# Optimization experiments

Hardware: AMD Instinct MI355X
Metric: run time of the kernel (lower is better)

Reference implementation:

```python
import jax, jax.numpy as jnp
import numpy as np


def _ln(x, g, b, eps=1e-5):
    m = x.mean(-1, keepdims=True)
    v = x.var(-1, keepdims=True)
    return (x - m) / jnp.sqrt(v + eps) * g + b


def setup_inputs() -> dict:
    key = jax.random.key(0)
    ks = jax.random.split(key, 12)
    B, N, F, D, DI = 1024, 100000, 128, 256, 512

    def w(k, shape, fan_in):
        return jax.random.normal(k, shape, jnp.float32) / np.sqrt(fan_in).astype(np.float32)

    return {
        "x_num": jax.random.normal(ks[0], (B, F), jnp.float32),
        "cand_num": jax.random.normal(ks[1], (N, F), jnp.float32),
        "cand_y": jax.random.normal(ks[2], (N, 1), jnp.float32),
        "W_lin": w(ks[3], (F, D), F), "b_lin": jnp.zeros(D, jnp.float32),
        "W_K": w(ks[4], (D, D), D), "b_K": jnp.zeros(D, jnp.float32),
        "W_Y": w(ks[5], (1, D), 2), "b_Y": jnp.zeros(D, jnp.float32),
        "W_T1": w(ks[6], (D, DI), D), "b_T1": jnp.zeros(DI, jnp.float32),
        "W_T2": w(ks[7], (DI, D), DI),
        "ln_p_g": jnp.ones(D, jnp.float32), "ln_p_b": jnp.zeros(D, jnp.float32),
        "W_P1": w(ks[8], (D, DI), D), "b_P1": jnp.zeros(DI, jnp.float32),
        "W_P2": w(ks[9], (DI, D), DI), "b_P2": jnp.zeros(D, jnp.float32),
        "ln_o_g": jnp.ones(D, jnp.float32), "ln_o_b": jnp.zeros(D, jnp.float32),
        "W_out": w(ks[10], (D, 1), D), "b_out": jnp.zeros(1, jnp.float32),
        "context_size": 96,
    }


def reference(x_num, cand_num, cand_y,
              W_lin, b_lin, W_K, b_K, W_Y, b_Y,
              W_T1, b_T1, W_T2,
              ln_p_g, ln_p_b, W_P1, b_P1, W_P2, b_P2,
              ln_o_g, ln_o_b, W_out, b_out,
              context_size):
    # Encoder (encoder_n_blocks=0, normlization=None -> identity f)
    x_enc = x_num @ W_lin + b_lin                       # [B, D]
    k = x_enc @ W_K + b_K                               # [B, D]
    # Candidate keys (computed under torch.no_grad in the original)
    ki_all = jax.lax.stop_gradient((cand_num @ W_lin + b_lin) @ W_K + b_K)  # [N, D]

    # Exact brute-force L2 kNN == faiss.IndexFlatL2
    d2 = (k * k).sum(-1, keepdims=True) - 2.0 * (k @ ki_all.T) + (ki_all * ki_all).sum(-1)  # [B, N]
    _, I = jax.lax.top_k(-d2, context_size)             # [B, C] ascending distance
    ki = ki_all[I]                                      # [B, C, D]

    # S = ||k - ki||^2 per the source formula; softmax over context
    S = (k * k).sum(-1, keepdims=True) \
        - 2.0 * jnp.einsum('bd,bcd->bc', k, ki) \
        + (ki * ki).sum(-1)                             # [B, C]
    weights = jax.nn.softmax(S, axis=-1)                # context_dropout=0 (eval)

    encode_y = cand_y[I] @ W_Y + b_Y                    # [B, C, D]
    diff = k[:, None, :] - ki                           # [B, C, D]
    V = encode_y + jax.nn.relu(diff @ W_T1 + b_T1) @ W_T2  # T MLP, no bias on 2nd linear
    V = jnp.einsum('bc,bcd->bd', weights, V)            # weighted context reduction

    x = x_enc + V
    # predictor residual block: LN -> Linear -> ReLU -> Linear
    h = _ln(x, ln_p_g, ln_p_b)
    x = x + (jax.nn.relu(h @ W_P1 + b_P1) @ W_P2 + b_P2)
    # head P: LN -> ReLU -> Linear(d, 1)
    return jax.nn.relu(_ln(x, ln_o_g, ln_o_b)) @ W_out + b_out  # [B, 1]
```

## Files before the change

### kernel.cpp

```cpp
#include <hip/hip_runtime.h>
#include <math.h>

#define BQ 1024
#define FDIM 128
#define DDIM 256
#define DIDIM 512
#define NTOT 100000
#define NP 100096
#define CTX 96
#define CAP 8192
#define MSUB 12288
#define RSUB 48
#define LBUF 1536
#define CSTR 16

typedef _Float16 f16x8 __attribute__((ext_vector_type(8)));
typedef _Float16 f16x4 __attribute__((ext_vector_type(4)));
typedef _Float16 f16x2 __attribute__((ext_vector_type(2)));
typedef float f32x4 __attribute__((ext_vector_type(4)));

__global__ __launch_bounds__(256) void k_fuse(
    const float* __restrict__ Wlin, const float* __restrict__ blin,
    const float* __restrict__ WK, const float* __restrict__ bK,
    float* __restrict__ Wf, float* __restrict__ bf)
{
    __shared__ float red[256];
    int i = blockIdx.x, j = threadIdx.x;
    if (i < FDIM) {
        float acc = 0.f;
        for (int l = 0; l < DDIM; ++l) acc += Wlin[i*DDIM + l] * WK[l*DDIM + j];
        Wf[i*DDIM + j] = acc;
    } else {
        float acc = bK[j];
        for (int l = 0; l < DDIM; ++l) acc += blin[l] * WK[l*DDIM + j];
        bf[j] = acc;
        red[j] = acc*acc; __syncthreads();
        for (int s2 = 128; s2 > 0; s2 >>= 1) { if (j < s2) red[j] += red[j+s2]; __syncthreads(); }
        if (j == 0) bf[256] = red[0];
    }
}

__global__ __launch_bounds__(256) void k_fuse2(
    const float* __restrict__ Wf, const float* __restrict__ WT1, float* __restrict__ WfT1)
{
    __shared__ float wr[DDIM];
    int i = blockIdx.x, j = threadIdx.x;
    wr[j] = Wf[i*DDIM + j];
    __syncthreads();
    float a0 = 0.f, a1 = 0.f;
    for (int l = 0; l < DDIM; ++l) {
        float w = wr[l];
        a0 += w * WT1[(size_t)l*DIDIM + j];
        a1 += w * WT1[(size_t)l*DIDIM + j + 256];
    }
    WfT1[(size_t)i*DIDIM + j] = a0;
    WfT1[(size_t)i*DIDIM + j + 256] = a1;
}

__global__ __launch_bounds__(128) void k_cvt_w(
    const float* __restrict__ Wf, const float* __restrict__ WfT1, _Float16* __restrict__ Wsp)
{
    int j = blockIdx.x, l = threadIdx.x;
    float w = (j < DDIM) ? Wf[l*DDIM + j] : WfT1[(size_t)l*DIDIM + (j - DDIM)];
    _Float16 h = (_Float16)w;
    float hf = (float)h;
    Wsp[(size_t)j*384 + l]       = h;
    Wsp[(size_t)j*384 + 128 + l] = (_Float16)((w - hf) * 64.f);
    Wsp[(size_t)j*384 + 256 + l] = (_Float16)(hf * 0.015625f);
}

__global__ __launch_bounds__(256) void k_query(
    const float* __restrict__ x, const float* __restrict__ Wlin,
    const float* __restrict__ blin, const float* __restrict__ Wf,
    const float* __restrict__ bf,
    float* __restrict__ xenc, float* __restrict__ kq)
{
    __shared__ float xs[FDIM];
    int b = blockIdx.x, j = threadIdx.x;
    if (j < FDIM) xs[j] = x[(size_t)b*FDIM + j];
    __syncthreads();
    float a0 = blin[j], a1 = bf[j];
    for (int l = 0; l < FDIM; ++l) {
        float xv = xs[l];
        a0 += xv * Wlin[l*DDIM + j];
        a1 += xv * Wf[l*DDIM + j];
    }
    xenc[(size_t)b*DDIM + j] = a0;
    kq[(size_t)b*DDIM + j] = a1;
}

__global__ __launch_bounds__(128) void k_kp(
    const float* __restrict__ kq, const float* __restrict__ Wf, float* __restrict__ kp)
{
    __shared__ float ks[DDIM];
    int b = blockIdx.x, l = threadIdx.x;
    ks[l] = kq[(size_t)b*DDIM + l];
    ks[l+128] = kq[(size_t)b*DDIM + l + 128];
    __syncthreads();
    float a = 0.f;
    for (int d = 0; d < DDIM; ++d) a += Wf[l*DDIM + d] * ks[d];
    kp[(size_t)b*FDIM + l] = a;
}

__global__ __launch_bounds__(256) void k_xp(
    const float* __restrict__ x, const float* __restrict__ WfT1,
    const float* __restrict__ bT1, float* __restrict__ xP)
{
    __shared__ float xs[FDIM];
    int b = blockIdx.x, j = threadIdx.x;
    if (j < FDIM) xs[j] = x[(size_t)b*FDIM + j];
    __syncthreads();
    float a0 = bT1[j], a1 = bT1[j + 256];
    for (int l = 0; l < FDIM; ++l) {
        float xv = xs[l];
        a0 += xv * WfT1[(size_t)l*DIDIM + j];
        a1 += xv * WfT1[(size_t)l*DIDIM + j + 256];
    }
    xP[(size_t)b*DIDIM + j] = a0;
    xP[(size_t)b*DIDIM + j + 256] = a1;
}

__global__ __launch_bounds__(256) void k_cvt_kp(
    const float* __restrict__ kp, _Float16* __restrict__ kp2)
{
    int t = blockIdx.x*256 + threadIdx.x;
    int row = t >> 5;
    int c4 = (t & 31) * 4;
    float4 v = *(const float4*)(kp + (size_t)row*FDIM + c4);
    float vv[4] = {v.x, v.y, v.z, v.w};
    f16x4 h, hs, l;
    #pragma unroll
    for (int q = 0; q < 4; ++q) {
        _Float16 hq = (_Float16)vv[q];
        float hf = (float)hq;
        h[q]  = hq;
        hs[q] = (_Float16)(hf * 0.015625f);
        l[q]  = (_Float16)((vv[q] - hf) * 64.f);
    }
    size_t b = (size_t)row*384 + c4;
    *(f16x4*)(kp2 + b)       = h;
    *(f16x4*)(kp2 + b + 128) = l;
    *(f16x4*)(kp2 + b + 256) = hs;
}

__global__ __launch_bounds__(256) void k_cvt_cand(
    const float* __restrict__ cand, _Float16* __restrict__ c2)
{
    int t = blockIdx.x*256 + threadIdx.x;
    int row = t >> 5;
    int c4 = (t & 31) * 4;
    float4 v = {0.f, 0.f, 0.f, 0.f};
    if (row < NTOT) v = *(const float4*)(cand + (size_t)row*FDIM + c4);
    float vv[4] = {v.x, v.y, v.z, v.w};
    f16x4 h, hs, l;
    #pragma unroll
    for (int q = 0; q < 4; ++q) {
        _Float16 hq = (_Float16)vv[q];
        float hf = (float)hq;
        h[q]  = hq;
        hs[q] = (_Float16)(hf * 0.015625f);
        l[q]  = (_Float16)((vv[q] - hf) * 64.f);
    }
    size_t b = (size_t)row*384 + c4;
    *(f16x4*)(c2 + b)       = h;
    *(f16x4*)(c2 + b + 128) = hs;
    *(f16x4*)(c2 + b + 256) = l;
}

__global__ __launch_bounds__(256) void k_cnorm(
    const _Float16* __restrict__ A, const _Float16* __restrict__ B,
    float* __restrict__ knp, const float* __restrict__ bf)
{
    __shared__ __align__(16) _Float16 As[128*64];
    __shared__ __align__(16) _Float16 Bs[128*64];
    int tid = threadIdx.x;
    int lane = tid & 63, wv = tid >> 6;
    int wm = wv >> 1, wn = wv & 1;
    int bn = blockIdx.x * 128;
    int bm = blockIdx.y * 128;
    f32x4 acc[4][4] = {};
    const size_t baseA = (size_t)bm * 384;
    const size_t baseB = (size_t)bn * 384;
    for (int kt = 0; kt < 6; ++kt) {
        #pragma unroll
        for (int r = 0; r < 4; ++r) {
            int w = wv*4 + r;
            int s = w*64 + lane;
            int rl = s & 15;
            int q  = (s >> 4) & 3;
            int kk2= (s >> 6) & 1;
            int ii = (s >> 7) & 3;
            int wq = (s >> 9) & 1;
            size_t goff = (size_t)(wq*64 + ii*16 + rl)*384 + kt*64 + (kk2*4 + q)*8;
            __builtin_amdgcn_global_load_lds(
                (const __attribute__((address_space(1))) void*)(A + baseA + goff),
                (__attribute__((address_space(3))) void*)(As + w*512), 16, 0, 0);
            __builtin_amdgcn_global_load_lds(
                (const __attribute__((address_space(1))) void*)(B + baseB + goff),
                (__attribute__((address_space(3))) void*)(Bs + w*512), 16, 0, 0);
        }
        __syncthreads();
        #pragma unroll
        for (int kk = 0; kk < 2; ++kk) {
            f16x8 af[4], bfr[4];
            #pragma unroll
            for (int i = 0; i < 4; ++i)
                af[i] = *(const f16x8*)&As[((wm*8 + i*2 + kk)*64 + (lane>>4)*16 + (lane&15))*8];
            #pragma unroll
            for (int j = 0; j < 4; ++j)
                bfr[j] = *(const f16x8*)&Bs[((wn*8 + j*2 + kk)*64 + (lane>>4)*16 + (lane&15))*8];
            #pragma unroll
            for (int i = 0; i < 4; ++i)
                #pragma unroll
                for (int j = 0; j < 4; ++j)
                    acc[i][j] = __builtin_amdgcn_mfma_f32_16x16x32_f16(af[i], bfr[j], acc[i][j], 0, 0, 0);
        }
        __syncthreads();
    }
    float bfv[4];
    #pragma unroll
    for (int j = 0; j < 4; ++j) bfv[j] = bf[bn + wn*64 + j*16 + (lane&15)];
    int bnt = bn >> 7;
    #pragma unroll
    for (int i = 0; i < 4; ++i) {
        #pragma unroll
        for (int rg = 0; rg < 4; ++rg) {
            float s = 0.f;
            #pragma unroll
            for (int j = 0; j < 4; ++j) {
                float q = acc[i][j][rg];
                s += q * (q + 2.f*bfv[j]);
            }
            s += __shfl_xor(s, 1, 64);
            s += __shfl_xor(s, 2, 64);
            s += __shfl_xor(s, 4, 64);
            s += __shfl_xor(s, 8, 64);
            if ((lane & 15) == 0) {
                int row = bm + wm*64 + i*16 + (lane>>4)*4 + rg;
                knp[(size_t)(bnt*2 + wn)*NP + row] = s;
            }
        }
    }
}

__global__ __launch_bounds__(256) void k_norm_fin(
    const float* __restrict__ knp, const float* __restrict__ bf, float* __restrict__ kinorm)
{
    int n = blockIdx.x*256 + threadIdx.x;
    kinorm[n] = (n < NTOT)
        ? bf[256] + knp[n] + knp[(size_t)NP + n] + knp[(size_t)2*NP + n] + knp[(size_t)3*NP + n]
        : INFINITY;
}

__global__ __launch_bounds__(256) void k_mini(
    const _Float16* __restrict__ kp2, const _Float16* __restrict__ cand2,
    const float* __restrict__ kinorm, _Float16* __restrict__ msb)
{
    __shared__ __align__(16) _Float16 As[128*64];
    __shared__ __align__(16) _Float16 Bs[128*64];
    int tid = threadIdx.x;
    int lane = tid & 63, wv = tid >> 6;
    int wm = wv >> 1, wn = wv & 1;
    int bm = blockIdx.x * 128;
    int bn = blockIdx.y * 128;
    f32x4 acc[4][4] = {};
    const size_t baseA = (size_t)bm * 384;
    const size_t baseB = (size_t)bn * 384;
    for (int kt = 0; kt < 2; ++kt) {
        #pragma unroll
        for (int r = 0; r < 4; ++r) {
            int w = wv*4 + r;
            int s = w*64 + lane;
            int rl = s & 15;
            int q  = (s >> 4) & 3;
            int kk2= (s >> 6) & 1;
            int ii = (s >> 7) & 3;
            int wq = (s >> 9) & 1;
            size_t goff = (size_t)(wq*64 + ii*16 + rl)*384 + kt*64 + (kk2*4 + q)*8;
            __builtin_amdgcn_global_load_lds(
                (const __attribute__((address_space(1))) void*)(kp2 + baseA + goff),
                (__attribute__((address_space(3))) void*)(As + w*512), 16, 0, 0);
            __builtin_amdgcn_global_load_lds(
                (const __attribute__((address_space(1))) void*)(cand2 + baseB + goff),
                (__attribute__((address_space(3))) void*)(Bs + w*512), 16, 0, 0);
        }
        __syncthreads();
        #pragma unroll
        for (int kk = 0; kk < 2; ++kk) {
            f16x8 af[4], bfr[4];
            #pragma unroll
            for (int i = 0; i < 4; ++i)
                af[i] = *(const f16x8*)&As[((wm*8 + i*2 + kk)*64 + (lane>>4)*16 + (lane&15))*8];
            #pragma unroll
            for (int j = 0; j < 4; ++j)
                bfr[j] = *(const f16x8*)&Bs[((wn*8 + j*2 + kk)*64 + (lane>>4)*16 + (lane&15))*8];
            #pragma unroll
            for (int i = 0; i < 4; ++i)
                #pragma unroll
                for (int j = 0; j < 4; ++j)
                    acc[i][j] = __builtin_amdgcn_mfma_f32_16x16x32_f16(af[i], bfr[j], acc[i][j], 0, 0, 0);
        }
        __syncthreads();
    }
    #pragma unroll
    for (int i = 0; i < 4; ++i) {
        int m = bm + wm*64 + i*16 + (lane>>4)*4;
        #pragma unroll
        for (int j = 0; j < 4; ++j) {
            int nl = bn + wn*64 + j*16 + (lane&15);
            float kn = kinorm[nl];
            #pragma unroll
            for (int rg = 0; rg < 4; ++rg)
                msb[(size_t)(m + rg)*MSUB + nl] = (_Float16)fmaxf(kn - 2.f*acc[i][j][rg], 0.f);
        }
    }
}

__global__ __launch_bounds__(256) void k_subT(
    const unsigned short* __restrict__ msb, int* __restrict__ Tq, int* __restrict__ cnt)
{
    __shared__ unsigned h[1024];
    __shared__ unsigned pr[256];
    __shared__ unsigned h2[64];
    __shared__ int tstar;
    __shared__ unsigned cbel;
    int b = blockIdx.x, tid = threadIdx.x;
    if (tid == 0) cnt[b*CSTR] = 0;
    #pragma unroll
    for (int i = 0; i < 4; ++i) h[tid + i*256] = 0;
    if (tid == 0) tstar = 1023;
    if (tid < 64) h2[tid] = 0;
    __syncthreads();
    const unsigned short* row = msb + (size_t)b*MSUB;
    for (int base = 0; base < MSUB; base += 2048) {
        uint4 u = *(const uint4*)(row + base + tid*8);
        atomicAdd(&h[(u.x & 0xffffu) >> 6], 1u);
        atomicAdd(&h[(u.x >> 16) >> 6], 1u);
        atomicAdd(&h[(u.y & 0xffffu) >> 6], 1u);
        atomicAdd(&h[(u.y >> 16) >> 6], 1u);
        atomicAdd(&h[(u.z & 0xffffu) >> 6], 1u);
        atomicAdd(&h[(u.z >> 16) >> 6], 1u);
        atomicAdd(&h[(u.w & 0xffffu) >> 6], 1u);
        atomicAdd(&h[(u.w >> 16) >> 6], 1u);
    }
    __syncthreads();
    unsigned s0 = h[tid*4], s1 = h[tid*4+1], s2 = h[tid*4+2], s3 = h[tid*4+3];
    unsigned tot = s0 + s1 + s2 + s3;
    pr[tid] = tot;
    __syncthreads();
    for (int off = 1; off < 256; off <<= 1) {
        unsigned t2 = (tid >= off) ? pr[tid - off] : 0;
        __syncthreads();
        pr[tid] += t2;
        __syncthreads();
    }
    unsigned c = pr[tid] - tot;
    int found = -1;
    c += s0; if (c >= RSUB) found = tid*4;
    if (found < 0) { c += s1; if (c >= RSUB) found = tid*4+1; }
    if (found < 0) { c += s2; if (c >= RSUB) found = tid*4+2; }
    if (found < 0) { c += s3; if (c >= RSUB) found = tid*4+3; }
    if (found >= 0) atomicMin(&tstar, found);
    __syncthreads();
    if (tid == (tstar >> 2)) {
        unsigned below = pr[tid] - tot;
        int pos = tstar & 3;
        if (pos > 0) below += s0;
        if (pos > 1) below += s1;
        if (pos > 2) below += s2;
        cbel = below;
    }
    __syncthreads();
    int ts = tstar;
    for (int base = 0; base < MSUB; base += 2048) {
        uint4 u = *(const uint4*)(row + base + tid*8);
        unsigned e[8] = { u.x & 0xffffu, u.x >> 16, u.y & 0xffffu, u.y >> 16,
                          u.z & 0xffffu, u.z >> 16, u.w & 0xffffu, u.w >> 16 };
        #pragma unroll
        for (int q = 0; q < 8; ++q)
            if ((int)(e[q] >> 6) == ts) atomicAdd(&h2[e[q] & 63], 1u);
    }
    __syncthreads();
    if (tid == 0) {
        unsigned cum = cbel; int code = 63;
        for (int i = 0; i < 64; ++i) { cum += h2[i]; if (cum >= RSUB) { code = i; break; } }
        Tq[b] = (ts << 6) + code;
    }
}

__global__ __launch_bounds__(256) void k_dist_mfma(
    const _Float16* __restrict__ kp2, const _Float16* __restrict__ cand2,
    const float* __restrict__ kinorm, const int* __restrict__ Tq,
    int* __restrict__ cnt, int* __restrict__ candI)
{
    __shared__ __align__(16) _Float16 As[128*64];
    __shared__ __align__(16) _Float16 Bs[128*64];
    __shared__ int lcnt;
    __shared__ unsigned lbuf[LBUF];
    int tid = threadIdx.x;
    int lane = tid & 63, wv = tid >> 6;
    int wm = wv >> 1, wn = wv & 1;
    int r0 = blockIdx.x & 7, u0 = blockIdx.x >> 3;
    int pq = r0*782 + u0;
    int bm = (pq & 7) * 128;
    int bn = (pq >> 3) * 128;
    if (tid == 0) lcnt = 0;
    f32x4 acc[4][4] = {};
    const size_t baseA = (size_t)bm * 384;
    const size_t baseB = (size_t)bn * 384;
    for (int kt = 0; kt < 2; ++kt) {
        #pragma unroll
        for (int r = 0; r < 4; ++r) {
            int w = wv*4 + r;
            int s = w*64 + lane;
            int rl = s & 15;
            int q  = (s >> 4) & 3;
            int kk2= (s >> 6) & 1;
            int ii = (s >> 7) & 3;
            int wq = (s >> 9) & 1;
            size_t goff = (size_t)(wq*64 + ii*16 + rl)*384 + kt*64 + (kk2*4 + q)*8;
            __builtin_amdgcn_global_load_lds(
                (const __attribute__((address_space(1))) void*)(kp2 + baseA + goff),
                (__attribute__((address_space(3))) void*)(As + w*512), 16, 0, 0);
            __builtin_amdgcn_global_load_lds(
                (const __attribute__((address_space(1))) void*)(cand2 + baseB + goff),
                (__attribute__((address_space(3))) void*)(Bs + w*512), 16, 0, 0);
        }
        __syncthreads();
        #pragma unroll
        for (int kk = 0; kk < 2; ++kk) {
            f16x8 af[4], bfr[4];
            #pragma unroll
            for (int i = 0; i < 4; ++i)
                af[i] = *(const f16x8*)&As[((wm*8 + i*2 + kk)*64 + (lane>>4)*16 + (lane&15))*8];
            #pragma unroll
            for (int j = 0; j < 4; ++j)
                bfr[j] = *(const f16x8*)&Bs[((wn*8 + j*2 + kk)*64 + (lane>>4)*16 + (lane&15))*8];
            #pragma unroll
            for (int i = 0; i < 4; ++i)
                #pragma unroll
                for (int j = 0; j < 4; ++j)
                    acc[i][j] = __builtin_amdgcn_mfma_f32_16x16x32_f16(af[i], bfr[j], acc[i][j], 0, 0, 0);
        }
        __syncthreads();
    }
    #pragma unroll
    for (int i = 0; i < 4; ++i) {
        int m0 = bm + wm*64 + i*16 + (lane>>4)*4;
        int tqs[4];
        #pragma unroll
        for (int rg = 0; rg < 4; ++rg) tqs[rg] = Tq[m0 + rg];
        #pragma unroll
        for (int j = 0; j < 4; ++j) {
            int nl = bn + wn*64 + j*16 + (lane&15);
            float kn = kinorm[nl];
            #pragma unroll
            for (int rg = 0; rg < 4; ++rg) {
                float sc = fmaxf(kn - 2.f*acc[i][j][rg], 0.f);
                _Float16 k16 = (_Float16)sc;
                unsigned short kb;
                __builtin_memcpy(&kb, &k16, 2);
                if (kb <= (unsigned short)tqs[rg]) {
                    int p = atomicAdd(&lcnt, 1);
                    if (p < LBUF) lbuf[p] = ((unsigned)(m0 + rg) << 17) | (unsigned)nl;
                    else {
                        int pp = atomicAdd(&cnt[(m0 + rg)*CSTR], 1);
                        if (pp < CAP) candI[(size_t)(m0 + rg)*CAP + pp] = nl;
                    }
                }
            }
        }
    }
    __syncthreads();
    int c = lcnt < LBUF ? lcnt : LBUF;
    for (int i2 = tid; i2 < c; i2 += 256) {
        unsigned pk = lbuf[i2];
        int row = pk >> 17, col = (int)(pk & 0x1ffffu);
        int pp = atomicAdd(&cnt[row*CSTR], 1);
        if (pp < CAP) candI[(size_t)row*CAP + pp] = col;
    }
}

__device__ __forceinline__ float row_score(
    const float* __restrict__ cand, const float* kps, const float* __restrict__ kinorm, int n)
{
    float acc0 = 0.f, acc1 = 0.f;
    #pragma unroll 4
    for (int d = 0; d < FDIM; d += 8) {
        float4 v0 = *(const float4*)(cand + (size_t)n*FDIM + d);
        float4 v1 = *(const float4*)(cand + (size_t)n*FDIM + d + 4);
        acc0 += v0.x*kps[d]   + v0.y*kps[d+1] + v0.z*kps[d+2] + v0.w*kps[d+3];
        acc1 += v1.x*kps[d+4] + v1.y*kps[d+5] + v1.z*kps[d+6] + v1.w*kps[d+7];
    }
    return kinorm[n] - 2.f*(acc0 + acc1);
}

__global__ __launch_bounds__(256) void k_fix(
    const float* __restrict__ kp, const float* __restrict__ cand,
    const float* __restrict__ kinorm, int* __restrict__ cnt, int* __restrict__ candI)
{
    __shared__ float kps[FDIM];
    __shared__ unsigned h[1024];
    __shared__ unsigned pr[256];
    __shared__ unsigned h2[64];
    __shared__ int tstar;
    __shared__ unsigned cbel;
    __shared__ unsigned Tsh;
    int b = blockIdx.x, tid = threadIdx.x;
    int c0 = cnt[b*CSTR];
    if (c0 >= CTX && c0 <= CAP) return;
    if (tid < FDIM) kps[tid] = kp[(size_t)b*FDIM + tid];
    #pragma unroll
    for (int i = 0; i < 4; ++i) h[tid + i*256] = 0;
    if (tid == 0) tstar = 1023;
    if (tid < 64) h2[tid] = 0;
    __syncthreads();
    for (int n = tid; n < NTOT; n += 256) {
        float sc = fmaxf(row_score(cand, kps, kinorm, n), 0.f);
        _Float16 k16 = (_Float16)sc;
        unsigned short kb; __builtin_memcpy(&kb, &k16, 2);
        atomicAdd(&h[kb >> 6], 1u);
    }
    __syncthreads();
    unsigned s0 = h[tid*4], s1 = h[tid*4+1], s2 = h[tid*4+2], s3 = h[tid*4+3];
    unsigned tot = s0 + s1 + s2 + s3;
    pr[tid] = tot;
    __syncthreads();
    for (int off = 1; off < 256; off <<= 1) {
        unsigned t2 = (tid >= off) ? pr[tid - off] : 0;
        __syncthreads();
        pr[tid] += t2;
        __syncthreads();
    }
    unsigned c = pr[tid] - tot;
    int found = -1;
    c += s0; if (c >= CTX) found = tid*4;
    if (found < 0) { c += s1; if (c >= CTX) found = tid*4+1; }
    if (found < 0) { c += s2; if (c >= CTX) found = tid*4+2; }
    if (found < 0) { c += s3; if (c >= CTX) found = tid*4+3; }
    if (found >= 0) atomicMin(&tstar, found);
    __syncthreads();
    if (tid == (tstar >> 2)) {
        unsigned below = pr[tid] - tot;
        int pos = tstar & 3;
        if (pos > 0) below += s0;
        if (pos > 1) below += s1;
        if (pos > 2) below += s2;
        cbel = below;
    }
    __syncthreads();
    int ts = tstar;
    for (int n = tid; n < NTOT; n += 256) {
        float sc = fmaxf(row_score(cand, kps, kinorm, n), 0.f);
        _Float16 k16 = (_Float16)sc;
        unsigned short kb; __builtin_memcpy(&kb, &k16, 2);
        if ((int)((unsigned)kb >> 6) == ts) atomicAdd(&h2[kb & 63], 1u);
    }
    __syncthreads();
    if (tid == 0) {
        unsigned cum = cbel; int code = 63;
        for (int i = 0; i < 64; ++i) { cum += h2[i]; if (cum >= CTX) { code = i; break; } }
        Tsh = (unsigned)((ts << 6) + code);
        cnt[b*CSTR] = 0;
    }
    __syncthreads();
    unsigned T2 = Tsh;
    for (int n = tid; n < NTOT; n += 256) {
        float sc = fmaxf(row_score(cand, kps, kinorm, n), 0.f);
        _Float16 k16 = (_Float16)sc;
        unsigned short kb; __builtin_memcpy(&kb, &k16, 2);
        if ((unsigned)kb <= T2) {
            int pp = atomicAdd(&cnt[b*CSTR], 1);
            if (pp < CAP) candI[(size_t)b*CAP + pp] = n;
        }
    }
}

__global__ __launch_bounds__(256) void k_resc(
    const float* __restrict__ kp, const float* __restrict__ cand,
    const float* __restrict__ kinorm, const int* __restrict__ cnt,
    const int* __restrict__ candI,
    float* __restrict__ finV, int* __restrict__ finI)
{
    __shared__ float kps[FDIM];
    __shared__ float sval[2048];
    __shared__ int   sidx[2048];
    int b = blockIdx.x, tid = threadIdx.x;
    if (tid < FDIM) kps[tid] = kp[(size_t)b*FDIM + tid];
    if (tid < 128) { sval[tid] = INFINITY; sidx[tid] = 0x7fffffff; }
    int nc = cnt[b*CSTR]; if (nc > CAP) nc = CAP;
    __syncthreads();
    for (int c0 = 0; c0 < nc; c0 += 1920) {
        int m = nc - c0; if (m > 1920) m = 1920;
        for (int c = tid; c < m; c += 256) {
            int n = candI[(size_t)b*CAP + c0 + c];
            sval[128 + c] = row_score(cand, kps, kinorm, n);
            sidx[128 + c] = n;
        }
        __syncthreads();
        int nv = 128 + m;
        int size = 256; while (size < nv) size <<= 1;
        for (int i2 = nv + tid; i2 < size; i2 += 256) { sval[i2] = INFINITY; sidx[i2] = 0x7fffffff; }
        __syncthreads();
        for (int k2 = 2; k2 <= size; k2 <<= 1) {
            for (int jj = k2 >> 1; jj > 0; jj >>= 1) {
                for (int i = tid; i < size; i += 256) {
                    int ix = i ^ jj;
                    if (ix > i) {
                        bool up = ((i & k2) == 0);
                        float a = sval[i], b2 = sval[ix];
                        int ia = sidx[i], ib = sidx[ix];
                        bool gt = (a > b2) || (a == b2 && ia > ib);
                        if (gt == up) {
                            sval[i] = b2; sval[ix] = a;
                            sidx[i] = ib; sidx[ix] = ia;
                        }
                    }
                }
                __syncthreads();
            }
        }
    }
    if (tid < CTX) { finV[(size_t)b*CTX + tid] = sval[tid]; finI[(size_t)b*CTX + tid] = sidx[tid]; }
}

__global__ __launch_bounds__(128) void k_weights(
    const float* __restrict__ finV, const int* __restrict__ finI,
    const float* __restrict__ candy, float* __restrict__ wts, float* __restrict__ wy)
{
    __shared__ float sh[128];
    int b = blockIdx.x, t = threadIdx.x;
    float v = (t < CTX) ? finV[b*CTX + t] : -INFINITY;
    sh[t] = v; __syncthreads();
    for (int s2 = 64; s2 > 0; s2 >>= 1) { if (t < s2) sh[t] = fmaxf(sh[t], sh[t+s2]); __syncthreads(); }
    float m = sh[0]; __syncthreads();
    float e = (t < CTX) ? expf(v - m) : 0.f;
    sh[t] = e; __syncthreads();
    for (int s2 = 64; s2 > 0; s2 >>= 1) { if (t < s2) sh[t] += sh[t+s2]; __syncthreads(); }
    float w = e / sh[0]; __syncthreads();
    if (t < CTX) wts[b*CTX + t] = w;
    float yv = (t < CTX) ? candy[finI[b*CTX + t]] : 0.f;
    sh[t] = w * yv; __syncthreads();
    for (int s2 = 64; s2 > 0; s2 >>= 1) { if (t < s2) sh[t] += sh[t+s2]; __syncthreads(); }
    if (t == 0) wy[b] = sh[0];
}

__global__ __launch_bounds__(256) void k_tmlp2(
    const _Float16* __restrict__ c2, const _Float16* __restrict__ Wsp,
    const float* __restrict__ xP,
    const int* __restrict__ finI, const float* __restrict__ wts,
    float* __restrict__ Hw)
{
    __shared__ __align__(16) _Float16 As[768*8];
    __shared__ __align__(16) _Float16 Bs[1024*8];
    __shared__ int   idx[CTX];
    __shared__ float wsh[CTX];
    int b = blockIdx.x, ct = blockIdx.y;
    int tid = threadIdx.x;
    int lane = tid & 63, wv = tid >> 6;
    if (tid < CTX) { idx[tid] = finI[b*CTX + tid]; wsh[tid] = wts[b*CTX + tid]; }
    __syncthreads();
    f32x4 acc[6][2] = {};
    const _Float16* Wbase = Wsp + (size_t)(DDIM + ct*128) * 384;
    for (int kt = 0; kt < 2; ++kt) {
        #pragma unroll
        for (int w = 0; w < 3; ++w) {
            int s = (wv*3 + w)*64 + lane;
            int rl = s & 15, q = (s >> 4) & 3, kk2 = (s >> 6) & 1, ii = s >> 7;
            int grow = idx[ii*16 + rl];
            __builtin_amdgcn_global_load_lds(
                (const __attribute__((address_space(1))) void*)(c2 + (size_t)grow*384 + kt*64 + (kk2*4 + q)*8),
                (__attribute__((address_space(3))) void*)(As + (size_t)s*8), 16, 0, 0);
        }
        #pragma unroll
        for (int w = 0; w < 4; ++w) {
            int s = (wv*4 + w)*64 + lane;
            int rl = s & 15, q = (s >> 4) & 3, kk2 = (s >> 6) & 1, jj = s >> 7;
            __builtin_amdgcn_global_load_lds(
                (const __attribute__((address_space(1))) void*)(Wbase + (size_t)(jj*16 + rl)*384 + kt*64 + (kk2*4 + q)*8),
                (__attribute__((address_space(3))) void*)(Bs + (size_t)s*8), 16, 0, 0);
        }
        __syncthreads();
        #pragma unroll
        for (int kk = 0; kk < 2; ++kk) {
            f16x8 bfr[2];
            #pragma unroll
            for (int j = 0; j < 2; ++j)
                bfr[j] = *(const f16x8*)&Bs[(((wv*2 + j)*2 + kk)*64 + (lane>>4)*16 + (lane&15))*8];
            #pragma unroll
            for (int i = 0; i < 6; ++i) {
                f16x8 af = *(const f16x8*)&As[((i*2 + kk)*64 + (lane>>4)*16 + (lane&15))*8];
                #pragma unroll
                for (int j = 0; j < 2; ++j)
                    acc[i][j] = __builtin_amdgcn_mfma_f32_16x16x32_f16(af, bfr[j], acc[i][j], 0, 0, 0);
            }
        }
        __syncthreads();
    }
    #pragma unroll
    for (int j = 0; j < 2; ++j) {
        int col = ct*128 + wv*32 + j*16 + (lane & 15);
        float xv = xP[(size_t)b*DIDIM + col];
        float p = 0.f;
        #pragma unroll
        for (int i = 0; i < 6; ++i) {
            #pragma unroll
            for (int rg = 0; rg < 4; ++rg) {
                int row = i*16 + (lane>>4)*4 + rg;
                p += wsh[row] * fmaxf(xv - acc[i][j][rg], 0.f);
            }
        }
        p += __shfl_xor(p, 16, 64);
        p += __shfl_xor(p, 32, 64);
        if ((lane >> 4) == 0) Hw[(size_t)b*DIDIM + col] = p;
    }
}

__device__ __forceinline__ float bsum(float v, float* red, int j)
{
    red[j] = v; __syncthreads();
    if (j < 64) {
        float t = red[j] + red[j+64] + red[j+128] + red[j+192];
        #pragma unroll
        for (int o2 = 32; o2; o2 >>= 1) t += __shfl_xor(t, o2, 64);
        if (j == 0) red[0] = t;
    }
    __syncthreads();
    float t = red[0];
    __syncthreads();
    return t;
}

__global__ __launch_bounds__(256) void k_final4(
    const float* __restrict__ xenc, const float* __restrict__ Hw,
    const float* __restrict__ wy,
    const float* __restrict__ WY, const float* __restrict__ bY,
    const float* __restrict__ WT2,
    const float* __restrict__ lpg, const float* __restrict__ lpb,
    const float* __restrict__ WP1, const float* __restrict__ bP1,
    const float* __restrict__ WP2, const float* __restrict__ bP2,
    const float* __restrict__ logg, const float* __restrict__ lob,
    const float* __restrict__ Wout, const float* __restrict__ bout,
    float* __restrict__ out)
{
    __shared__ float hs[4][DIDIM];
    __shared__ float xs[4][DDIM];
    __shared__ float red[256];
    int b0 = blockIdx.x*4, j = threadIdx.x;
    #pragma unroll
    for (int r = 0; r < 4; ++r) {
        hs[r][j] = Hw[(size_t)(b0+r)*DIDIM + j];
        hs[r][j+256] = Hw[(size_t)(b0+r)*DIDIM + j + 256];
    }
    __syncthreads();
    float v[4];
    #pragma unroll
    for (int r = 0; r < 4; ++r) v[r] = wy[b0+r]*WY[j] + bY[j];
    for (int dd = 0; dd < DIDIM; ++dd) {
        float w = WT2[dd*DDIM + j];
        #pragma unroll
        for (int r = 0; r < 4; ++r) v[r] += hs[r][dd]*w;
    }
    float x[4];
    #pragma unroll
    for (int r = 0; r < 4; ++r) x[r] = xenc[(size_t)(b0+r)*DDIM + j] + v[r];
    #pragma unroll
    for (int r = 0; r < 4; ++r) {
        float mean = bsum(x[r], red, j) * (1.f/DDIM);
        float xc = x[r] - mean;
        float var = bsum(xc*xc, red, j) * (1.f/DDIM);
        float rstd = 1.f / sqrtf(var + 1e-5f);
        xs[r][j] = xc * rstd * lpg[j] + lpb[j];
    }
    __syncthreads();
    float u0[4], u1[4];
    #pragma unroll
    for (int r = 0; r < 4; ++r) { u0[r] = bP1[j]; u1[r] = bP1[j+256]; }
    for (int dd = 0; dd < DDIM; ++dd) {
        float w0 = WP1[(size_t)dd*DIDIM + j], w1 = WP1[(size_t)dd*DIDIM + j + 256];
        #pragma unroll
        for (int r = 0; r < 4; ++r) { float hd = xs[r][dd]; u0[r] += hd*w0; u1[r] += hd*w1; }
    }
    __syncthreads();
    #pragma unroll
    for (int r = 0; r < 4; ++r) { hs[r][j] = fmaxf(u0[r], 0.f); hs[r][j+256] = fmaxf(u1[r], 0.f); }
    __syncthreads();
    float x2[4];
    #pragma unroll
    for (int r = 0; r < 4; ++r) x2[r] = x[r] + bP2[j];
    for (int dd = 0; dd < DIDIM; ++dd) {
        float w = WP2[dd*DDIM + j];
        #pragma unroll
        for (int r = 0; r < 4; ++r) x2[r] += hs[r][dd]*w;
    }
    #pragma unroll
    for (int r = 0; r < 4; ++r) {
        float mean = bsum(x2[r], red, j) * (1.f/DDIM);
        float xc = x2[r] - mean;
        float var = bsum(xc*xc, red, j) * (1.f/DDIM);
        float rstd = 1.f / sqrtf(var + 1e-5f);
        float rr = fmaxf(xc * rstd * logg[j] + lob[j], 0.f);
        float s = bsum(rr * Wout[j], red, j);
        if (j == 0) out[b0+r] = s + bout[0];
    }
}

extern "C" void kernel_launch(void* const* d_in, const int* in_sizes, int n_in,
                              void* d_out, int out_size, void* d_ws, size_t ws_size,
                              hipStream_t stream)
{
    (void)in_sizes; (void)n_in; (void)out_size; (void)ws_size;
    const float* x_num = (const float*)d_in[0];
    const float* cand  = (const float*)d_in[1];
    const float* candy = (const float*)d_in[2];
    const float* Wlin  = (const float*)d_in[3];
    const float* blin  = (const float*)d_in[4];
    const float* WK    = (const float*)d_in[5];
    const float* bK    = (const float*)d_in[6];
    const float* WY    = (const float*)d_in[7];
    const float* bY    = (const float*)d_in[8];
    const float* WT1   = (const float*)d_in[9];
    const float* bT1   = (const float*)d_in[10];
    const float* WT2   = (const float*)d_in[11];
    const float* lpg   = (const float*)d_in[12];
    const float* lpb   = (const float*)d_in[13];
    const float* WP1   = (const float*)d_in[14];
    const float* bP1   = (const float*)d_in[15];
    const float* WP2   = (const float*)d_in[16];
    const float* bP2   = (const float*)d_in[17];
    const float* logg  = (const float*)d_in[18];
    const float* lob   = (const float*)d_in[19];
    const float* Wout  = (const float*)d_in[20];
    const float* bout  = (const float*)d_in[21];
    float* out = (float*)d_out;

    float* ws = (float*)d_ws;
    size_t o = 0;
    float* Wf     = ws + o; o += (size_t)FDIM*DDIM;
    float* bf     = ws + o; o += 320;
    float* WfT1   = ws + o; o += (size_t)FDIM*DIDIM;
    float* xenc   = ws + o; o += (size_t)BQ*DDIM;
    float* kq     = ws + o; o += (size_t)BQ*DDIM;
    float* kp     = ws + o; o += (size_t)BQ*FDIM;
    float* kinorm = ws + o; o += NP;
    float* knp    = ws + o; o += (size_t)4*NP;
    float* finV   = ws + o; o += (size_t)BQ*CTX;
    int*   finI   = (int*)(ws + o); o += (size_t)BQ*CTX;
    float* wts    = ws + o; o += (size_t)BQ*CTX;
    float* wy     = ws + o; o += BQ;
    int*   Tq     = (int*)(ws + o); o += BQ;
    float* Hw     = ws + o; o += (size_t)BQ*DIDIM;
    float* xP     = ws + o; o += (size_t)BQ*DIDIM;
    _Float16* kp2 = (_Float16*)(ws + o); o += (size_t)BQ*384/2;
    _Float16* c2  = (_Float16*)(ws + o); o += (size_t)NP*384/2;
    _Float16* Wsp = (_Float16*)(ws + o); o += (size_t)768*384/2;
    int*   cnt    = (int*)(ws + o); o += (size_t)BQ*CSTR;
    int*   candI  = (int*)(ws + o); o += (size_t)BQ*CAP;
    _Float16* msb = (_Float16*)(ws + o); o += (size_t)BQ*MSUB;

    k_fuse<<<dim3(FDIM+1), dim3(256), 0, stream>>>(Wlin, blin, WK, bK, Wf, bf);
    k_fuse2<<<dim3(FDIM), dim3(256), 0, stream>>>(Wf, WT1, WfT1);
    k_cvt_w<<<dim3(DDIM+DIDIM), dim3(128), 0, stream>>>(Wf, WfT1, Wsp);
    k_query<<<dim3(BQ), dim3(256), 0, stream>>>(x_num, Wlin, blin, Wf, bf, xenc, kq);
    k_kp<<<dim3(BQ), dim3(128), 0, stream>>>(kq, Wf, kp);
    k_xp<<<dim3(BQ), dim3(256), 0, stream>>>(x_num, WfT1, bT1, xP);
    k_cvt_kp<<<dim3(BQ*FDIM/4/256), dim3(256), 0, stream>>>(kp, kp2);
    k_cvt_cand<<<dim3(NP*FDIM/4/256), dim3(256), 0, stream>>>(cand, c2);

    k_cnorm<<<dim3(DDIM/128, NP/128), dim3(256), 0, stream>>>(c2, Wsp, knp, bf);
    k_norm_fin<<<dim3(NP/256), dim3(256), 0, stream>>>(knp, bf, kinorm);

    k_mini<<<dim3(BQ/128, MSUB/128), dim3(256), 0, stream>>>(kp2, c2, kinorm, msb);
    k_subT<<<dim3(BQ), dim3(256), 0, stream>>>((const unsigned short*)msb, Tq, cnt);

    k_dist_mfma<<<dim3((BQ/128)*(NP/128)), dim3(256), 0, stream>>>(kp2, c2, kinorm, Tq, cnt, candI);
    k_fix<<<dim3(BQ), dim3(256), 0, stream>>>(kp, cand, kinorm, cnt, candI);
    k_resc<<<dim3(BQ), dim3(256), 0, stream>>>(kp, cand, kinorm, cnt, candI, finV, finI);

    k_weights<<<dim3(BQ), dim3(128), 0, stream>>>(finV, finI, candy, wts, wy);

    k_tmlp2<<<dim3(BQ, 4), dim3(256), 0, stream>>>(c2, Wsp, xP, finI, wts, Hw);
    k_final4<<<dim3(BQ/4), dim3(256), 0, stream>>>(xenc, Hw, wy, WY, bY, WT2,
                                                   lpg, lpb, WP1, bP1, WP2, bP2,
                                                   logg, lob, Wout, bout, out);
}
```

Baseline: 441.5 us.

## Fuse query-side kernels, widen cnorm tile, merge softmax weights into rescoring

Four small per-query kernels (query encode, kp projection, xP projection, fp16 split of kp) are merged into one kernel, with kq kept in shared memory instead of a global buffer. The candidate-norm GEMM now has each block cover all 256 output columns, so the A tile is loaded once and only two partial-norm planes are written and summed. The softmax-weights kernel is folded into the rescoring kernel, dropping the finV buffer and one launch. Together these aim to remove launch overhead and redundant global traffic. The cost is more accumulator registers in cnorm, which may lower occupancy.

```diff
diff --git a/kernel.cpp b/kernel.cpp
--- a/kernel.cpp
+++ b/kernel.cpp
@@ -69,13 +69,16 @@
     Wsp[(size_t)j*384 + 256 + l] = (_Float16)(hf * 0.015625f);
 }
 
-__global__ __launch_bounds__(256) void k_query(
+__global__ __launch_bounds__(256) void k_qenc(
     const float* __restrict__ x, const float* __restrict__ Wlin,
     const float* __restrict__ blin, const float* __restrict__ Wf,
-    const float* __restrict__ bf,
-    float* __restrict__ xenc, float* __restrict__ kq)
+    const float* __restrict__ bf, const float* __restrict__ WfT1,
+    const float* __restrict__ bT1,
+    float* __restrict__ xenc, float* __restrict__ kp,
+    _Float16* __restrict__ kp2, float* __restrict__ xP)
 {
     __shared__ float xs[FDIM];
+    __shared__ float ks[DDIM];
     int b = blockIdx.x, j = threadIdx.x;
     if (j < FDIM) xs[j] = x[(size_t)b*FDIM + j];
     __syncthreads();
@@ -86,61 +89,26 @@
         a1 += xv * Wf[l*DDIM + j];
     }
     xenc[(size_t)b*DDIM + j] = a0;
-    kq[(size_t)b*DDIM + j] = a1;
-}
-
-__global__ __launch_bounds__(128) void k_kp(
-    const float* __restrict__ kq, const float* __restrict__ Wf, float* __restrict__ kp)
-{
-    __shared__ float ks[DDIM];
-    int b = blockIdx.x, l = threadIdx.x;
-    ks[l] = kq[(size_t)b*DDIM + l];
-    ks[l+128] = kq[(size_t)b*DDIM + l + 128];
-    __syncthreads();
-    float a = 0.f;
-    for (int d = 0; d < DDIM; ++d) a += Wf[l*DDIM + d] * ks[d];
-    kp[(size_t)b*FDIM + l] = a;
-}
-
-__global__ __launch_bounds__(256) void k_xp(
-    const float* __restrict__ x, const float* __restrict__ WfT1,
-    const float* __restrict__ bT1, float* __restrict__ xP)
-{
-    __shared__ float xs[FDIM];
-    int b = blockIdx.x, j = threadIdx.x;
-    if (j < FDIM) xs[j] = x[(size_t)b*FDIM + j];
-    __syncthreads();
-    float a0 = bT1[j], a1 = bT1[j + 256];
+    ks[j] = a1;
+    float p0 = bT1[j], p1 = bT1[j + 256];
     for (int l = 0; l < FDIM; ++l) {
         float xv = xs[l];
-        a0 += xv * WfT1[(size_t)l*DIDIM + j];
-        a1 += xv * WfT1[(size_t)l*DIDIM + j + 256];
-    }
-    xP[(size_t)b*DIDIM + j] = a0;
-    xP[(size_t)b*DIDIM + j + 256] = a1;
-}
-
-__global__ __launch_bounds__(256) void k_cvt_kp(
-    const float* __restrict__ kp, _Float16* __restrict__ kp2)
-{
-    int t = blockIdx.x*256 + threadIdx.x;
-    int row = t >> 5;
-    int c4 = (t & 31) * 4;
-    float4 v = *(const float4*)(kp + (size_t)row*FDIM + c4);
-    float vv[4] = {v.x, v.y, v.z, v.w};
-    f16x4 h, hs, l;
-    #pragma unroll
-    for (int q = 0; q < 4; ++q) {
-        _Float16 hq = (_Float16)vv[q];
-        float hf = (float)hq;
-        h[q]  = hq;
-        hs[q] = (_Float16)(hf * 0.015625f);
-        l[q]  = (_Float16)((vv[q] - hf) * 64.f);
-    }
-    size_t b = (size_t)row*384 + c4;
-    *(f16x4*)(kp2 + b)       = h;
-    *(f16x4*)(kp2 + b + 128) = l;
-    *(f16x4*)(kp2 + b + 256) = hs;
+        p0 += xv * WfT1[(size_t)l*DIDIM + j];
+        p1 += xv * WfT1[(size_t)l*DIDIM + j + 256];
+    }
+    xP[(size_t)b*DIDIM + j] = p0;
+    xP[(size_t)b*DIDIM + j + 256] = p1;
+    __syncthreads();
+    if (j < FDIM) {
+        float a = 0.f;
+        for (int d = 0; d < DDIM; ++d) a += Wf[j*DDIM + d] * ks[d];
+        kp[(size_t)b*FDIM + j] = a;
+        _Float16 h = (_Float16)a;
+        float hf = (float)h;
+        kp2[(size_t)b*384 + j]       = h;
+        kp2[(size_t)b*384 + 128 + j] = (_Float16)((a - hf) * 64.f);
+        kp2[(size_t)b*384 + 256 + j] = (_Float16)(hf * 0.015625f);
+    }
 }
 
 __global__ __launch_bounds__(256) void k_cvt_cand(
@@ -172,62 +140,58 @@
     float* __restrict__ knp, const float* __restrict__ bf)
 {
     __shared__ __align__(16) _Float16 As[128*64];
-    __shared__ __align__(16) _Float16 Bs[128*64];
+    __shared__ __align__(16) _Float16 Bs[2][128*64];
     int tid = threadIdx.x;
     int lane = tid & 63, wv = tid >> 6;
     int wm = wv >> 1, wn = wv & 1;
-    int bn = blockIdx.x * 128;
-    int bm = blockIdx.y * 128;
-    f32x4 acc[4][4] = {};
+    int bm = blockIdx.x * 128;
+    f32x4 acc[4][8] = {};
     const size_t baseA = (size_t)bm * 384;
-    const size_t baseB = (size_t)bn * 384;
     for (int kt = 0; kt < 6; ++kt) {
         #pragma unroll
         for (int r = 0; r < 4; ++r) {
             int w = wv*4 + r;
             int s = w*64 + lane;
-            int rl = s & 15;
-            int q  = (s >> 4) & 3;
-            int kk2= (s >> 6) & 1;
-            int ii = (s >> 7) & 3;
-            int wq = (s >> 9) & 1;
+            int rl = s & 15, q = (s>>4)&3, kk2 = (s>>6)&1, ii = (s>>7)&3, wq = (s>>9)&1;
             size_t goff = (size_t)(wq*64 + ii*16 + rl)*384 + kt*64 + (kk2*4 + q)*8;
             __builtin_amdgcn_global_load_lds(
                 (const __attribute__((address_space(1))) void*)(A + baseA + goff),
                 (__attribute__((address_space(3))) void*)(As + w*512), 16, 0, 0);
-            __builtin_amdgcn_global_load_lds(
-                (const __attribute__((address_space(1))) void*)(B + baseB + goff),
-                (__attribute__((address_space(3))) void*)(Bs + w*512), 16, 0, 0);
+            #pragma unroll
+            for (int t = 0; t < 2; ++t) {
+                size_t goffB = (size_t)(t*128 + wq*64 + ii*16 + rl)*384 + kt*64 + (kk2*4 + q)*8;
+                __builtin_amdgcn_global_load_lds(
+                    (const __attribute__((address_space(1))) void*)(B + goffB),
+                    (__attribute__((address_space(3))) void*)(Bs[t] + w*512), 16, 0, 0);
+            }
         }
         __syncthreads();
         #pragma unroll
         for (int kk = 0; kk < 2; ++kk) {
-            f16x8 af[4], bfr[4];
+            f16x8 af[4];
             #pragma unroll
             for (int i = 0; i < 4; ++i)
                 af[i] = *(const f16x8*)&As[((wm*8 + i*2 + kk)*64 + (lane>>4)*16 + (lane&15))*8];
             #pragma unroll
-            for (int j = 0; j < 4; ++j)
-                bfr[j] = *(const f16x8*)&Bs[((wn*8 + j*2 + kk)*64 + (lane>>4)*16 + (lane&15))*8];
-            #pragma unroll
-            for (int i = 0; i < 4; ++i)
+            for (int j = 0; j < 8; ++j) {
+                f16x8 bfr = *(const f16x8*)&Bs[wn][((j*2 + kk)*64 + (lane>>4)*16 + (lane&15))*8];
                 #pragma unroll
-                for (int j = 0; j < 4; ++j)
-                    acc[i][j] = __builtin_amdgcn_mfma_f32_16x16x32_f16(af[i], bfr[j], acc[i][j], 0, 0, 0);
-        }
-        __syncthreads();
-    }
-    float bfv[4];
-    #pragma unroll
-    for (int j = 0; j < 4; ++j) bfv[j] = bf[bn + wn*64 + j*16 + (lane&15)];
-    int bnt = bn >> 7;
+                for (int i = 0; i < 4; ++i)
+                    acc[i][j] = __builtin_amdgcn_mfma_f32_16x16x32_f16(af[i], bfr, acc[i][j], 0, 0, 0);
+            }
+        }
+        __syncthreads();
+    }
+    float bfv[8];
+    #pragma unroll
+    for (int j = 0; j < 8; ++j) bfv[j] = bf[wn*128 + j*16 + (lane&15)];
     #pragma unroll
     for (int i = 0; i < 4; ++i) {
         #pragma unroll
         for (int rg = 0; rg < 4; ++rg) {
             float s = 0.f;
             #pragma unroll
-            for (int j = 0; j < 4; ++j) {
+            for (int j = 0; j < 8; ++j) {
                 float q = acc[i][j][rg];
                 s += q * (q + 2.f*bfv[j]);
             }
@@ -237,7 +201,7 @@
             s += __shfl_xor(s, 8, 64);
             if ((lane & 15) == 0) {
                 int row = bm + wm*64 + i*16 + (lane>>4)*4 + rg;
-                knp[(size_t)(bnt*2 + wn)*NP + row] = s;
+                knp[(size_t)wn*NP + row] = s;
             }
         }
     }
@@ -248,7 +212,7 @@
 {
     int n = blockIdx.x*256 + threadIdx.x;
     kinorm[n] = (n < NTOT)
-        ? bf[256] + knp[n] + knp[(size_t)NP + n] + knp[(size_t)2*NP + n] + knp[(size_t)3*NP + n]
+        ? bf[256] + knp[n] + knp[(size_t)NP + n]
         : INFINITY;
 }
 
@@ -579,12 +543,13 @@
 __global__ __launch_bounds__(256) void k_resc(
     const float* __restrict__ kp, const float* __restrict__ cand,
     const float* __restrict__ kinorm, const int* __restrict__ cnt,
-    const int* __restrict__ candI,
-    float* __restrict__ finV, int* __restrict__ finI)
+    const int* __restrict__ candI, const float* __restrict__ candy,
+    int* __restrict__ finI, float* __restrict__ wts, float* __restrict__ wy)
 {
     __shared__ float kps[FDIM];
     __shared__ float sval[2048];
     __shared__ int   sidx[2048];
+    __shared__ float sh[256];
     int b = blockIdx.x, tid = threadIdx.x;
     if (tid < FDIM) kps[tid] = kp[(size_t)b*FDIM + tid];
     if (tid < 128) { sval[tid] = INFINITY; sidx[tid] = 0x7fffffff; }
@@ -621,28 +586,20 @@
             }
         }
     }
-    if (tid < CTX) { finV[(size_t)b*CTX + tid] = sval[tid]; finI[(size_t)b*CTX + tid] = sidx[tid]; }
-}
-
-__global__ __launch_bounds__(128) void k_weights(
-    const float* __restrict__ finV, const int* __restrict__ finI,
-    const float* __restrict__ candy, float* __restrict__ wts, float* __restrict__ wy)
-{
-    __shared__ float sh[128];
-    int b = blockIdx.x, t = threadIdx.x;
-    float v = (t < CTX) ? finV[b*CTX + t] : -INFINITY;
-    sh[t] = v; __syncthreads();
-    for (int s2 = 64; s2 > 0; s2 >>= 1) { if (t < s2) sh[t] = fmaxf(sh[t], sh[t+s2]); __syncthreads(); }
-    float m = sh[0]; __syncthreads();
-    float e = (t < CTX) ? expf(v - m) : 0.f;
-    sh[t] = e; __syncthreads();
-    for (int s2 = 64; s2 > 0; s2 >>= 1) { if (t < s2) sh[t] += sh[t+s2]; __syncthreads(); }
-    float w = e / sh[0]; __syncthreads();
-    if (t < CTX) wts[b*CTX + t] = w;
-    float yv = (t < CTX) ? candy[finI[b*CTX + t]] : 0.f;
-    sh[t] = w * yv; __syncthreads();
-    for (int s2 = 64; s2 > 0; s2 >>= 1) { if (t < s2) sh[t] += sh[t+s2]; __syncthreads(); }
-    if (t == 0) wy[b] = sh[0];
+    if (tid < CTX) finI[(size_t)b*CTX + tid] = sidx[tid];
+    float m = sval[CTX-1];
+    float e = (tid < CTX) ? expf(sval[tid] - m) : 0.f;
+    sh[tid] = e;
+    __syncthreads();
+    for (int s2 = 128; s2 > 0; s2 >>= 1) { if (tid < s2) sh[tid] += sh[tid+s2]; __syncthreads(); }
+    float sum = sh[0];
+    __syncthreads();
+    float w = e / sum;
+    if (tid < CTX) wts[(size_t)b*CTX + tid] = w;
+    sh[tid] = (tid < CTX) ? w * candy[sidx[tid]] : 0.f;
+    __syncthreads();
+    for (int s2 = 128; s2 > 0; s2 >>= 1) { if (tid < s2) sh[tid] += sh[tid+s2]; __syncthreads(); }
+    if (tid == 0) wy[b] = sh[0];
 }
 
 __global__ __launch_bounds__(256) void k_tmlp2(
@@ -840,11 +797,9 @@
     float* bf     = ws + o; o += 320;
     float* WfT1   = ws + o; o += (size_t)FDIM*DIDIM;
     float* xenc   = ws + o; o += (size_t)BQ*DDIM;
-    float* kq     = ws + o; o += (size_t)BQ*DDIM;
     float* kp     = ws + o; o += (size_t)BQ*FDIM;
     float* kinorm = ws + o; o += NP;
-    float* knp    = ws + o; o += (size_t)4*NP;
-    float* finV   = ws + o; o += (size_t)BQ*CTX;
+    float* knp    = ws + o; o += (size_t)2*NP;
     int*   finI   = (int*)(ws + o); o += (size_t)BQ*CTX;
     float* wts    = ws + o; o += (size_t)BQ*CTX;
     float* wy     = ws + o; o += BQ;
@@ -861,13 +816,11 @@
     k_fuse<<<dim3(FDIM+1), dim3(256), 0, stream>>>(Wlin, blin, WK, bK, Wf, bf);
     k_fuse2<<<dim3(FDIM), dim3(256), 0, stream>>>(Wf, WT1, WfT1);
     k_cvt_w<<<dim3(DDIM+DIDIM), dim3(128), 0, stream>>>(Wf, WfT1, Wsp);
-    k_query<<<dim3(BQ), dim3(256), 0, stream>>>(x_num, Wlin, blin, Wf, bf, xenc, kq);
-    k_kp<<<dim3(BQ), dim3(128), 0, stream>>>(kq, Wf, kp);
-    k_xp<<<dim3(BQ), dim3(256), 0, stream>>>(x_num, WfT1, bT1, xP);
-    k_cvt_kp<<<dim3(BQ*FDIM/4/256), dim3(256), 0, stream>>>(kp, kp2);
+    k_qenc<<<dim3(BQ), dim3(256), 0, stream>>>(x_num, Wlin, blin, Wf, bf, WfT1, bT1,
+                                               xenc, kp, kp2, xP);
     k_cvt_cand<<<dim3(NP*FDIM/4/256), dim3(256), 0, stream>>>(cand, c2);
 
-    k_cnorm<<<dim3(DDIM/128, NP/128), dim3(256), 0, stream>>>(c2, Wsp, knp, bf);
+    k_cnorm<<<dim3(NP/128), dim3(256), 0, stream>>>(c2, Wsp, knp, bf);
     k_norm_fin<<<dim3(NP/256), dim3(256), 0, stream>>>(knp, bf, kinorm);
 
     k_mini<<<dim3(BQ/128, MSUB/128), dim3(256), 0, stream>>>(kp2, c2, kinorm, msb);
@@ -875,9 +828,8 @@
 
     k_dist_mfma<<<dim3((BQ/128)*(NP/128)), dim3(256), 0, stream>>>(kp2, c2, kinorm, Tq, cnt, candI);
     k_fix<<<dim3(BQ), dim3(256), 0, stream>>>(kp, cand, kinorm, cnt, candI);
-    k_resc<<<dim3(BQ), dim3(256), 0, stream>>>(kp, cand, kinorm, cnt, candI, finV, finI);
-
-    k_weights<<<dim3(BQ), dim3(128), 0, stream>>>(finV, finI, candy, wts, wy);
+    k_resc<<<dim3(BQ), dim3(256), 0, stream>>>(kp, cand, kinorm, cnt, candI, candy,
+                                               finI, wts, wy);
 
     k_tmlp2<<<dim3(BQ, 4), dim3(256), 0, stream>>>(c2, Wsp, xP, finI, wts, Hw);
     k_final4<<<dim3(BQ/4), dim3(256), 0, stream>>>(xenc, Hw, wy, WY, bY, WT2,
```

Result: slower. 452.6 us (+2.5%).
